# Optimization experiments

Measured on AMD Instinct MI355X. Metric: run time of the kernel, lower is better.

## Reference

```python
import jax, jax.numpy as jnp
import numpy as np

N_NODES = 50000
N_EDGES = 800000
IN_FEATS = 256
OUT_FEATS = 64
NUM_HEADS = 4
NEG_SLOPE = 0.2


def setup_inputs() -> dict:
    key = jax.random.key(0)
    k1, k2, k3, k4, k5, k6 = jax.random.split(key, 6)
    feat = jax.random.normal(k1, (N_NODES, IN_FEATS), dtype=jnp.float32)
    src = jax.random.randint(k2, (N_EDGES,), 0, N_NODES, dtype=jnp.int32)
    dst = jax.random.randint(k3, (N_EDGES,), 0, N_NODES, dtype=jnp.int32)
    # fc weight (no bias), xavier-like scale
    W = jax.random.normal(k4, (IN_FEATS, NUM_HEADS * OUT_FEATS), dtype=jnp.float32) * 0.05
    attn_l = jax.random.normal(k5, (NUM_HEADS, OUT_FEATS), dtype=jnp.float32) * 0.1
    attn_r = jax.random.normal(k6, (NUM_HEADS, OUT_FEATS), dtype=jnp.float32) * 0.1
    return {"feat": feat, "src": src, "dst": dst, "W": W, "attn_l": attn_l, "attn_r": attn_r}


def reference(feat, src, dst, W, attn_l, attn_r):
    N = feat.shape[0]
    # fc: [N, H*F] -> [N, H, F]
    ft = (feat @ W).reshape(N, NUM_HEADS, OUT_FEATS)
    # per-node attention logits [N, H]
    el = jnp.einsum('nhf,hf->nh', ft, attn_l)
    er = jnp.einsum('nhf,hf->nh', ft, attn_r)
    # edge logits: u_add_v then leaky relu  [E, H]
    e = el[src] + er[dst]
    e = jnp.where(e > 0, e, NEG_SLOPE * e)
    # edge softmax over edges sharing the same dst, numerically stable
    m = jax.ops.segment_max(e, dst, num_segments=N)          # [N, H]
    e_exp = jnp.exp(e - m[dst])                               # [E, H]
    denom = jax.ops.segment_sum(e_exp, dst, num_segments=N)  # [N, H]
    a = e_exp / denom[dst]                                    # [E, H]
    # u_mul_e + sum: gather src features, weight, scatter-add to dst
    msg = ft[src] * a[:, :, None]                             # [E, H, F]
    out = jax.ops.segment_sum(msg, dst, num_segments=N)      # [N, H, F]
    return out
```

## Files before the change

kernel.cpp:

```cpp
#include <hip/hip_runtime.h>
#include <hip/hip_bf16.h>
#include <math.h>

#define N_NODES 50000
#define N_EDGES 800000
#define IN_F 256
#define HF 256
#define NHEAD 4
#define OF 64
#define NPAD 50176
#define CAP 96
#define BM 192
#define MPAD 50304

typedef __attribute__((ext_vector_type(8))) short short8;
typedef __attribute__((ext_vector_type(4))) float f32x4;

__device__ __forceinline__ ushort f32_to_bf16(float x) {
  unsigned u = __float_as_uint(x);
  u += 0x7FFFu + ((u >> 16) & 1u);
  return (ushort)(u >> 16);
}
__device__ __forceinline__ float bfl(unsigned u) { return __uint_as_float(u << 16); }
__device__ __forceinline__ float bfh(unsigned u) { return __uint_as_float(u & 0xFFFF0000u); }

__device__ __forceinline__ void gload_lds16(const void* g, void* l) {
  __builtin_amdgcn_global_load_lds(
      (const __attribute__((address_space(1))) unsigned int*)g,
      (__attribute__((address_space(3))) unsigned int*)l, 16, 0, 0);
}

__global__ __launch_bounds__(256) void prep(const float* __restrict__ W,
                                            ushort* __restrict__ WT,
                                            int* __restrict__ cnt) {
  int i = blockIdx.x * blockDim.x + threadIdx.x;
  int stride = gridDim.x * blockDim.x;
  for (int j = i; j < IN_F * HF; j += stride) {
    int n = j >> 8, k = j & 255;
    WT[j] = f32_to_bf16(W[k * HF + n]);
  }
  for (int j = i; j < NPAD; j += stride) cnt[j] = 0;
}

__global__ __launch_bounds__(512) void gemm_f32a(const float* __restrict__ A,
                                                 const ushort* __restrict__ BT,
                                                 const float* __restrict__ al,
                                                 const float* __restrict__ ar,
                                                 ushort* __restrict__ C,
                                                 float* __restrict__ el,
                                                 float* __restrict__ er) {
  __shared__ char lds[40960];
  char* As = lds;
  char* Bs = lds + 24576;
  int tid = threadIdx.x;
  int w = tid >> 6, lane = tid & 63;
  int wm = w >> 2;
  int hq = w & 3;
  int brow = blockIdx.x * BM;
  int rl = lane & 15, khalf = lane >> 4;
  f32x4 acc[6][4];
#pragma unroll
  for (int m = 0; m < 6; ++m)
#pragma unroll
    for (int n = 0; n < 4; ++n) acc[m][n] = (f32x4){0.f, 0.f, 0.f, 0.f};

  for (int k0 = 0; k0 < IN_F; k0 += 32) {
#pragma unroll
    for (int part = 0; part < 3; ++part) {
      int ii = w * 3 + part;
      int d = ii * 1024 + lane * 16;
      int trow = d >> 7;
      int slot = (d >> 4) & 7;
      int srcslot = slot ^ (trow & 7);
      int ga = min(brow + trow, N_NODES - 1);
      gload_lds16(A + (size_t)ga * IN_F + k0 + srcslot * 4, As + d);
    }
#pragma unroll
    for (int part = 0; part < 2; ++part) {
      int ii = w * 2 + part;
      int d = ii * 1024 + lane * 16;
      int trow = d >> 6;
      int slot = (d >> 4) & 3;
      int srcslot = slot ^ ((trow >> 1) & 3);
      gload_lds16(BT + (size_t)trow * IN_F + k0 + srcslot * 8, Bs + d);
    }
    __syncthreads();
    short8 a[6], b[4];
#pragma unroll
    for (int m = 0; m < 6; ++m) {
      int r = wm * 96 + m * 16 + rl;
      int s0 = khalf * 2, s1 = khalf * 2 + 1;
      float4 lo = *(const float4*)(As + r * 128 + ((s0 ^ (r & 7)) << 4));
      float4 hi = *(const float4*)(As + r * 128 + ((s1 ^ (r & 7)) << 4));
      union { short8 s; unsigned u[4]; } cv;
      cv.u[0] = __builtin_amdgcn_perm(__float_as_uint(lo.y), __float_as_uint(lo.x), 0x07060302);
      cv.u[1] = __builtin_amdgcn_perm(__float_as_uint(lo.w), __float_as_uint(lo.z), 0x07060302);
      cv.u[2] = __builtin_amdgcn_perm(__float_as_uint(hi.y), __float_as_uint(hi.x), 0x07060302);
      cv.u[3] = __builtin_amdgcn_perm(__float_as_uint(hi.w), __float_as_uint(hi.z), 0x07060302);
      a[m] = cv.s;
    }
#pragma unroll
    for (int n = 0; n < 4; ++n) {
      int c = hq * 64 + n * 16 + rl;
      b[n] = *(const short8*)(Bs + c * 64 + ((khalf ^ ((c >> 1) & 3)) << 4));
    }
#pragma unroll
    for (int m = 0; m < 6; ++m)
#pragma unroll
      for (int n = 0; n < 4; ++n)
        acc[m][n] = __builtin_amdgcn_mfma_f32_16x16x32_bf16(a[m], b[n], acc[m][n], 0, 0, 0);
    __syncthreads();
  }

#pragma unroll
  for (int m = 0; m < 6; ++m) {
    int r0 = brow + wm * 96 + m * 16 + khalf * 4;
#pragma unroll
    for (int n = 0; n < 4; ++n) {
      int col = hq * 64 + n * 16 + rl;
#pragma unroll
      for (int j = 0; j < 4; ++j)
        C[(size_t)(r0 + j) * HF + col] = f32_to_bf16(acc[m][n][j]);
    }
  }

  float alv[4], arv[4];
#pragma unroll
  for (int n = 0; n < 4; ++n) {
    alv[n] = al[hq * OF + n * 16 + rl];
    arv[n] = ar[hq * OF + n * 16 + rl];
  }
#pragma unroll
  for (int m = 0; m < 6; ++m) {
    int r0 = brow + wm * 96 + m * 16 + khalf * 4;
#pragma unroll
    for (int j = 0; j < 4; ++j) {
      float pl = acc[m][0][j] * alv[0] + acc[m][1][j] * alv[1] +
                 acc[m][2][j] * alv[2] + acc[m][3][j] * alv[3];
      float pr = acc[m][0][j] * arv[0] + acc[m][1][j] * arv[1] +
                 acc[m][2][j] * arv[2] + acc[m][3][j] * arv[3];
#pragma unroll
      for (int off2 = 1; off2 < 16; off2 <<= 1) {
        pl += __shfl_xor(pl, off2);
        pr += __shfl_xor(pr, off2);
      }
      int r = r0 + j;
      if (rl == 0 && r < N_NODES) {
        el[r * NHEAD + hq] = pl;
        er[r * NHEAD + hq] = pr;
      }
    }
  }
}

__global__ __launch_bounds__(256) void fill_fixed(const int* __restrict__ src,
                                                  const int* __restrict__ dst,
                                                  int* __restrict__ cnt,
                                                  int* __restrict__ csr_src) {
  int stride = gridDim.x * blockDim.x;
  for (int e = blockIdx.x * blockDim.x + threadIdx.x; e < N_EDGES; e += stride) {
    int s = __builtin_nontemporal_load(&src[e]);
    int d = dst[e];
    int p = atomicAdd(&cnt[d], 1);
    if (p < CAP) csr_src[d * CAP + p] = s;
  }
}

__global__ __launch_bounds__(256) void aggregate(const int* __restrict__ cnt,
                                                 const int* __restrict__ csr_src,
                                                 const float* __restrict__ el,
                                                 const float* __restrict__ er,
                                                 const ushort* __restrict__ ft,
                                                 float* __restrict__ out) {
  int w = threadIdx.x >> 6, lane = threadIdx.x & 63;
  int n = blockIdx.x * 4 + w;
  if (n >= N_NODES) return;
  int half = lane >> 5, l5 = lane & 31;
  int h = l5 >> 3;
  int c = l5 << 3;
  float erh = er[n * NHEAD + h];
  int j0 = n * CAP;
  int j1 = j0 + min(cnt[n], CAP);
  float a0 = 0.f, a1 = 0.f, a2 = 0.f, a3 = 0.f;
  float a4 = 0.f, a5 = 0.f, a6 = 0.f, a7 = 0.f;
  float den = 0.f;
#pragma unroll 4
  for (int j = j0 + half; j < j1; j += 2) {
    int s = __builtin_nontemporal_load(&csr_src[j]);
    float x = el[s * NHEAD + h] + erh;
    x = x > 0.f ? x : 0.2f * x;
    float a = __expf(x);
    den += a;
    uint4 u = *(const uint4*)(ft + (size_t)s * HF + c);
    a0 += bfl(u.x) * a; a1 += bfh(u.x) * a;
    a2 += bfl(u.y) * a; a3 += bfh(u.y) * a;
    a4 += bfl(u.z) * a; a5 += bfh(u.z) * a;
    a6 += bfl(u.w) * a; a7 += bfh(u.w) * a;
  }
  den += __shfl_xor(den, 32);
  a0 += __shfl_xor(a0, 32); a1 += __shfl_xor(a1, 32);
  a2 += __shfl_xor(a2, 32); a3 += __shfl_xor(a3, 32);
  a4 += __shfl_xor(a4, 32); a5 += __shfl_xor(a5, 32);
  a6 += __shfl_xor(a6, 32); a7 += __shfl_xor(a7, 32);
  if (half == 0) {
    float inv = den > 0.f ? 1.0f / den : 0.f;
    f32x4 r0 = {a0 * inv, a1 * inv, a2 * inv, a3 * inv};
    f32x4 r1 = {a4 * inv, a5 * inv, a6 * inv, a7 * inv};
    __builtin_nontemporal_store(r0, (f32x4*)&out[(size_t)n * HF + c]);
    __builtin_nontemporal_store(r1, (f32x4*)&out[(size_t)n * HF + c + 4]);
  }
}

extern "C" void kernel_launch(void* const* d_in, const int* in_sizes, int n_in,
                              void* d_out, int out_size, void* d_ws, size_t ws_size,
                              hipStream_t stream) {
  const float* feat = (const float*)d_in[0];
  const int*   src  = (const int*)d_in[1];
  const int*   dst  = (const int*)d_in[2];
  const float* W    = (const float*)d_in[3];
  const float* al   = (const float*)d_in[4];
  const float* ar   = (const float*)d_in[5];
  float* out = (float*)d_out;

  char* ws = (char*)d_ws;
  ushort* ft_bf   = (ushort*)(ws);
  int*    csr_src = (int*)(ws + 26000000);
  int*    cnt     = (int*)(ws + 45400000);
  float*  el      = (float*)(ws + 45700000);
  float*  er      = (float*)(ws + 46500000);
  ushort* WT      = (ushort*)(ws + 47300000);

  prep<<<512, 256, 0, stream>>>(W, WT, cnt);
  gemm_f32a<<<MPAD / BM, 512, 0, stream>>>(feat, WT, al, ar, ft_bf, el, er);
  fill_fixed<<<3125, 256, 0, stream>>>(src, dst, cnt, csr_src);
  aggregate<<<(N_NODES + 3) / 4, 256, 0, stream>>>(cnt, csr_src, el, er, ft_bf, out);
}
```

Before: 161.1 us.

## Fuse GEMM and edge-bucketing into one launch with smaller GEMM tiles

Merges the projection GEMM and the edge bucketing (atomic count plus CSR fill) into a single kernel whose grid is split by block index. GEMM blocks now cover 64 rows with 256 threads instead of 192 rows with 512, and the trailing blocks run the edge scatter. This is meant to overlap the memory- and atomic-bound fill with the compute-bound GEMM and to drop one kernel launch. In exchange, the smaller tiles reload B more often per row and use less reuse, and the two workloads now compete for the same CUs.

```diff
diff --git a/kernel.cpp b/kernel.cpp
--- a/kernel.cpp
+++ b/kernel.cpp
@@ -10,8 +10,9 @@
 #define OF 64
 #define NPAD 50176
 #define CAP 96
-#define BM 192
-#define MPAD 50304
+#define MPAD 50048
+#define GEMM_BLOCKS 782
+#define FILL_BLOCKS 1250
 
 typedef __attribute__((ext_vector_type(8))) short short8;
 typedef __attribute__((ext_vector_type(4))) float f32x4;
@@ -42,32 +43,47 @@
   for (int j = i; j < NPAD; j += stride) cnt[j] = 0;
 }
 
-__global__ __launch_bounds__(512) void gemm_f32a(const float* __restrict__ A,
-                                                 const ushort* __restrict__ BT,
-                                                 const float* __restrict__ al,
-                                                 const float* __restrict__ ar,
-                                                 ushort* __restrict__ C,
-                                                 float* __restrict__ el,
-                                                 float* __restrict__ er) {
-  __shared__ char lds[40960];
+__global__ __launch_bounds__(256) void fused_gf(const float* __restrict__ A,
+                                                const ushort* __restrict__ BT,
+                                                const float* __restrict__ al,
+                                                const float* __restrict__ ar,
+                                                ushort* __restrict__ C,
+                                                float* __restrict__ el,
+                                                float* __restrict__ er,
+                                                const int* __restrict__ src,
+                                                const int* __restrict__ dst,
+                                                int* __restrict__ cnt,
+                                                int* __restrict__ csr_src) {
+  __shared__ char lds[24576];
+  int tid = threadIdx.x;
+
+  if (blockIdx.x >= GEMM_BLOCKS) {
+    int fb = blockIdx.x - GEMM_BLOCKS;
+    int stride = FILL_BLOCKS * 256;
+    for (int e = fb * 256 + tid; e < N_EDGES; e += stride) {
+      int s = __builtin_nontemporal_load(&src[e]);
+      int d = dst[e];
+      int p = atomicAdd(&cnt[d], 1);
+      if (p < CAP) csr_src[d * CAP + p] = s;
+    }
+    return;
+  }
+
   char* As = lds;
-  char* Bs = lds + 24576;
-  int tid = threadIdx.x;
+  char* Bs = lds + 8192;
   int w = tid >> 6, lane = tid & 63;
-  int wm = w >> 2;
-  int hq = w & 3;
-  int brow = blockIdx.x * BM;
+  int brow = blockIdx.x * 64;
   int rl = lane & 15, khalf = lane >> 4;
-  f32x4 acc[6][4];
-#pragma unroll
-  for (int m = 0; m < 6; ++m)
+  f32x4 acc[4][4];
+#pragma unroll
+  for (int m = 0; m < 4; ++m)
 #pragma unroll
     for (int n = 0; n < 4; ++n) acc[m][n] = (f32x4){0.f, 0.f, 0.f, 0.f};
 
   for (int k0 = 0; k0 < IN_F; k0 += 32) {
 #pragma unroll
-    for (int part = 0; part < 3; ++part) {
-      int ii = w * 3 + part;
+    for (int part = 0; part < 2; ++part) {
+      int ii = w * 2 + part;
       int d = ii * 1024 + lane * 16;
       int trow = d >> 7;
       int slot = (d >> 4) & 7;
@@ -76,8 +92,8 @@
       gload_lds16(A + (size_t)ga * IN_F + k0 + srcslot * 4, As + d);
     }
 #pragma unroll
-    for (int part = 0; part < 2; ++part) {
-      int ii = w * 2 + part;
+    for (int part = 0; part < 4; ++part) {
+      int ii = w * 4 + part;
       int d = ii * 1024 + lane * 16;
       int trow = d >> 6;
       int slot = (d >> 4) & 3;
@@ -85,10 +101,10 @@
       gload_lds16(BT + (size_t)trow * IN_F + k0 + srcslot * 8, Bs + d);
     }
     __syncthreads();
-    short8 a[6], b[4];
-#pragma unroll
-    for (int m = 0; m < 6; ++m) {
-      int r = wm * 96 + m * 16 + rl;
+    short8 a[4], b[4];
+#pragma unroll
+    for (int m = 0; m < 4; ++m) {
+      int r = m * 16 + rl;
       int s0 = khalf * 2, s1 = khalf * 2 + 1;
       float4 lo = *(const float4*)(As + r * 128 + ((s0 ^ (r & 7)) << 4));
       float4 hi = *(const float4*)(As + r * 128 + ((s1 ^ (r & 7)) << 4));
@@ -101,11 +117,11 @@
     }
 #pragma unroll
     for (int n = 0; n < 4; ++n) {
-      int c = hq * 64 + n * 16 + rl;
+      int c = w * 64 + n * 16 + rl;
       b[n] = *(const short8*)(Bs + c * 64 + ((khalf ^ ((c >> 1) & 3)) << 4));
     }
 #pragma unroll
-    for (int m = 0; m < 6; ++m)
+    for (int m = 0; m < 4; ++m)
 #pragma unroll
       for (int n = 0; n < 4; ++n)
         acc[m][n] = __builtin_amdgcn_mfma_f32_16x16x32_bf16(a[m], b[n], acc[m][n], 0, 0, 0);
@@ -113,11 +129,11 @@
   }
 
 #pragma unroll
-  for (int m = 0; m < 6; ++m) {
-    int r0 = brow + wm * 96 + m * 16 + khalf * 4;
+  for (int m = 0; m < 4; ++m) {
+    int r0 = brow + m * 16 + khalf * 4;
 #pragma unroll
     for (int n = 0; n < 4; ++n) {
-      int col = hq * 64 + n * 16 + rl;
+      int col = w * 64 + n * 16 + rl;
 #pragma unroll
       for (int j = 0; j < 4; ++j)
         C[(size_t)(r0 + j) * HF + col] = f32_to_bf16(acc[m][n][j]);
@@ -127,12 +143,12 @@
   float alv[4], arv[4];
 #pragma unroll
   for (int n = 0; n < 4; ++n) {
-    alv[n] = al[hq * OF + n * 16 + rl];
-    arv[n] = ar[hq * OF + n * 16 + rl];
-  }
-#pragma unroll
-  for (int m = 0; m < 6; ++m) {
-    int r0 = brow + wm * 96 + m * 16 + khalf * 4;
+    alv[n] = al[w * OF + n * 16 + rl];
+    arv[n] = ar[w * OF + n * 16 + rl];
+  }
+#pragma unroll
+  for (int m = 0; m < 4; ++m) {
+    int r0 = brow + m * 16 + khalf * 4;
 #pragma unroll
     for (int j = 0; j < 4; ++j) {
       float pl = acc[m][0][j] * alv[0] + acc[m][1][j] * alv[1] +
@@ -146,23 +162,10 @@
       }
       int r = r0 + j;
       if (rl == 0 && r < N_NODES) {
-        el[r * NHEAD + hq] = pl;
-        er[r * NHEAD + hq] = pr;
+        el[r * NHEAD + w] = pl;
+        er[r * NHEAD + w] = pr;
       }
     }
-  }
-}
-
-__global__ __launch_bounds__(256) void fill_fixed(const int* __restrict__ src,
-                                                  const int* __restrict__ dst,
-                                                  int* __restrict__ cnt,
-                                                  int* __restrict__ csr_src) {
-  int stride = gridDim.x * blockDim.x;
-  for (int e = blockIdx.x * blockDim.x + threadIdx.x; e < N_EDGES; e += stride) {
-    int s = __builtin_nontemporal_load(&src[e]);
-    int d = dst[e];
-    int p = atomicAdd(&cnt[d], 1);
-    if (p < CAP) csr_src[d * CAP + p] = s;
   }
 }
 
@@ -231,7 +234,7 @@
   ushort* WT      = (ushort*)(ws + 47300000);
 
   prep<<<512, 256, 0, stream>>>(W, WT, cnt);
-  gemm_f32a<<<MPAD / BM, 512, 0, stream>>>(feat, WT, al, ar, ft_bf, el, er);
-  fill_fixed<<<3125, 256, 0, stream>>>(src, dst, cnt, csr_src);
+  fused_gf<<<GEMM_BLOCKS + FILL_BLOCKS, 256, 0, stream>>>(feat, WT, al, ar, ft_bf,
+                                                          el, er, src, dst, cnt, csr_src);
   aggregate<<<(N_NODES + 3) / 4, 256, 0, stream>>>(cnt, csr_src, el, er, ft_bf, out);
 }
```

After: 150.3 us. 6.7% less time.
